# Performance work log

Measured on AMD Instinct MI355X. Metric: run time of the kernel, lower is better.

Reference implementation:

```python
import jax, jax.numpy as jnp
import numpy as np

N = 10000        # num_nodes
IN_DIM = 128     # in_dim
HID = 256        # hidden_size
EMB = 128        # final embedding dim
R = 8            # num_relations (== num_bases)
C = 32           # num_classes
E = 640000       # num_edges


def setup_inputs() -> dict:
    key = jax.random.key(0)
    ks = jax.random.split(key, 12)
    s = 0.05
    return {
        "x": jax.random.normal(ks[0], (N, N), jnp.float32) * s,
        "edge_index": jax.random.randint(ks[1], (2, E), 0, N),
        "edge_type": jax.random.randint(ks[2], (E,), 0, R),
        "emb": jax.random.normal(ks[3], (N, IN_DIM), jnp.float32) * s,
        "comp1": jax.random.normal(ks[4], (R, R), jnp.float32) * s,
        "basis1": jax.random.normal(ks[5], (R, IN_DIM, HID), jnp.float32) * s,
        "root1": jax.random.normal(ks[6], (IN_DIM, HID), jnp.float32) * s,
        "bias1": jnp.zeros((HID,), jnp.float32),
        "comp2": jax.random.normal(ks[7], (R, R), jnp.float32) * s,
        "basis2": jax.random.normal(ks[8], (R, HID, EMB), jnp.float32) * s,
        "root2": jax.random.normal(ks[9], (HID, EMB), jnp.float32) * s,
        "bias2": jnp.zeros((EMB,), jnp.float32),
        "w_dec": jax.random.normal(ks[10], (EMB, C), jnp.float32) * s,
    }


def _rgcn(h, src, dst, edge_type, comp, basis, root, bias):
    # basis-decomposed RGCN layer with mean aggregation (PyG RGCNConv semantics)
    # transform node features by every basis once: [N, B, out]
    hb = jnp.einsum("ni,bio->nbo", h, basis)
    # per-edge relation coefficients: [E, B]; message = comp[r] . hb[src]
    msg = jnp.einsum("eb,ebo->eo", comp[edge_type], hb[src])
    agg = jax.ops.segment_sum(msg, dst, num_segments=N)
    deg = jax.ops.segment_sum(jnp.ones((msg.shape[0],), h.dtype), dst, num_segments=N)
    agg = agg / jnp.maximum(deg, 1.0)[:, None]
    return agg + h @ root + bias


def reference(x, edge_index, edge_type, emb, comp1, basis1, root1, bias1,
              comp2, basis2, root2, bias2, w_dec):
    src, dst = edge_index[0], edge_index[1]
    h = jax.nn.relu(x @ emb)
    h = jax.nn.relu(_rgcn(h, src, dst, edge_type, comp1, basis1, root1, bias1))
    h = jax.nn.relu(_rgcn(h, src, dst, edge_type, comp2, basis2, root2, bias2))
    # multi-class inner-product decoder: logits = z @ W, softmax over classes
    return jax.nn.softmax(h @ w_dec, axis=1)
```

## Files before the change

kernel.cpp:

```cpp
#include <hip/hip_runtime.h>

typedef unsigned short u16;
typedef unsigned int u32;
typedef __attribute__((ext_vector_type(8))) short bf16x8;
typedef __attribute__((ext_vector_type(4))) float f32x4;

#define N_NODES 10000
#define E_EDGES 640000

static __device__ __forceinline__ float b2f(u16 u) {
  union { u32 i; float f; } x; x.i = ((u32)u) << 16; return x.f;
}
static __device__ __forceinline__ u16 f2b(float f) {
  union { float f; u32 i; } x; x.f = f;
  u32 r = x.i + 0x7FFF + ((x.i >> 16) & 1);
  return (u16)(r >> 16);
}
static __device__ __forceinline__ float ldf(const void* p, size_t i, int f32) {
  return f32 ? ((const float*)p)[i] : b2f(((const u16*)p)[i]);
}

__global__ __launch_bounds__(256) void detect_kernel(const u16* __restrict__ x, int* __restrict__ flag) {
  __shared__ int cnt_s;
  if (threadIdx.x == 0) cnt_s = 0;
  __syncthreads();
  int c = 0;
  for (int i = threadIdx.x; i < 4096; i += 256) {
    int e = (x[i] >> 7) & 255;
    if (e >= 140) c++;
  }
  atomicAdd(&cnt_s, c);
  __syncthreads();
  if (threadIdx.x == 0) flag[0] = (cnt_s > 64) ? 1 : 0;
}

__global__ void hist_kernel(const int* __restrict__ ei, const int* __restrict__ et,
                            int E, int* __restrict__ cnt8) {
  int e = blockIdx.x * 256 + threadIdx.x;
  if (e < E) atomicAdd(&cnt8[ei[E + e] * 8 + et[e]], 1);
}

__global__ void sumdst_kernel(const int* __restrict__ cnt8, int* __restrict__ dstcnt, int N) {
  int d = blockIdx.x * 256 + threadIdx.x;
  if (d >= N) return;
  const int4* p = (const int4*)(cnt8 + d * 8);
  int4 a = p[0], b = p[1];
  dstcnt[d] = a.x + a.y + a.z + a.w + b.x + b.y + b.z + b.w;
}

__global__ __launch_bounds__(256) void scan_kernel(const int* __restrict__ cnt,
                                                   int* __restrict__ offs,
                                                   int* __restrict__ cursor, int N) {
  __shared__ int tmp[256];
  const int t = threadIdx.x;
  const int CH = (N + 255) / 256;
  const int base = t * CH;
  int s = 0;
  for (int j = 0; j < CH; j++) { int p = base + j; if (p < N) s += cnt[p]; }
  tmp[t] = s;
  __syncthreads();
  for (int od = 1; od < 256; od <<= 1) {
    int a = (t >= od) ? tmp[t - od] : 0;
    __syncthreads();
    tmp[t] += a;
    __syncthreads();
  }
  int run = tmp[t] - s;
  for (int j = 0; j < CH; j++) {
    int p = base + j;
    if (p < N) { offs[p] = run; cursor[p] = run; run += cnt[p]; }
  }
  if (t == 255) offs[N] = tmp[255];
}

__global__ void segoffs_kernel(const int* __restrict__ dstoffs, const int* __restrict__ cnt8,
                               int* __restrict__ offs, int* __restrict__ cursor, int N) {
  int d = blockIdx.x * 256 + threadIdx.x;
  if (d >= N) return;
  int base = dstoffs[d];
  #pragma unroll
  for (int r = 0; r < 8; r++) {
    offs[d * 8 + r] = base;
    cursor[d * 8 + r] = base;
    base += cnt8[d * 8 + r];
  }
  if (d == N - 1) offs[N * 8] = base;
}

__global__ void bucket_kernel(const int* __restrict__ ei, const int* __restrict__ et,
                              int E, int* __restrict__ cursor, int* __restrict__ bucket) {
  int e = blockIdx.x * 256 + threadIdx.x;
  if (e < E) {
    int seg = ei[E + e] * 8 + et[e];
    int pos = atomicAdd(&cursor[seg], 1);
    bucket[pos] = ei[e];
  }
}

__global__ void transpose_kernel(const void* __restrict__ in, u16* __restrict__ out,
                                 int R, int C, const int* __restrict__ dflag) {
  __shared__ u16 tile[64][65];
  const int f = dflag[0];
  int r0 = blockIdx.x * 64, c0 = blockIdx.y * 64;
  int t = threadIdx.x;
  #pragma unroll
  for (int k = 0; k < 16; k++) {
    int lin = t + k * 256; int rr = lin >> 6, cc = lin & 63;
    int gr = r0 + rr;
    tile[rr][cc] = (gr < R) ? f2b(ldf(in, (size_t)gr * C + c0 + cc, f)) : (u16)0;
  }
  __syncthreads();
  #pragma unroll
  for (int k = 0; k < 16; k++) {
    int lin = t + k * 256; int rr = lin >> 6, cc = lin & 63;
    int gc = r0 + cc;
    if (gc < R) out[(size_t)(c0 + rr) * R + gc] = tile[cc][rr];
  }
}

template<int I, int O>
__global__ void wprep_kernel(const void* __restrict__ comp, const void* __restrict__ basis,
                             const void* __restrict__ root, u16* __restrict__ WT,
                             const int* __restrict__ dflag) {
  const int Kcat = 9 * I;
  const int f = dflag[0];
  int idx = blockIdx.x * 256 + threadIdx.x;
  if (idx >= Kcat * O) return;
  int o = idx % O;
  int kc = idx / O;
  float v;
  if (kc < 8 * I) {
    int r = kc / I, i = kc % I;
    float s = 0.f;
    #pragma unroll
    for (int b = 0; b < 8; b++)
      s += ldf(comp, r * 8 + b, f) * ldf(basis, ((size_t)b * I + i) * O + o, f);
    v = s;
  } else {
    int i = kc - 8 * I;
    v = ldf(root, (size_t)i * O + o, f);
  }
  WT[(size_t)o * Kcat + kc] = f2b(v);
}

template<int I>
__global__ void gather_seg_kernel(const u16* __restrict__ h, const int* __restrict__ offs,
                                  const int* __restrict__ bucket, u16* __restrict__ s, int node0) {
  const int d = node0 + blockIdx.x, t = threadIdx.x;
  const int sb = d * 8;
  const int b0 = offs[sb], bend = offs[sb + 8];
  const float inv = 1.0f / (float)((bend - b0) > 1 ? (bend - b0) : 1);
  const size_t base = (size_t)blockIdx.x * (9 * I);
  #pragma unroll
  for (int r = 0; r < 8; r++) {
    int j = offs[sb + r], j1 = offs[sb + r + 1];
    float a0 = 0.f, a1 = 0.f, a2 = 0.f, a3 = 0.f;
    for (; j + 3 < j1; j += 4) {
      int s0 = bucket[j], s1 = bucket[j + 1], s2 = bucket[j + 2], s3 = bucket[j + 3];
      a0 += b2f(h[(size_t)s0 * I + t]);
      a1 += b2f(h[(size_t)s1 * I + t]);
      a2 += b2f(h[(size_t)s2 * I + t]);
      a3 += b2f(h[(size_t)s3 * I + t]);
    }
    for (; j < j1; ++j) a0 += b2f(h[(size_t)bucket[j] * I + t]);
    s[base + r * I + t] = f2b((a0 + a1 + a2 + a3) * inv);
  }
  s[base + 8 * I + t] = h[(size_t)d * I + t];
}

__global__ __launch_bounds__(256) void gemm_kernel(
    const void* __restrict__ A, int lda,
    const u16* __restrict__ BT, int ldbt,
    int M, int Nout, int K,
    int tiles_per_split, int ktiles_total,
    float* __restrict__ partials,
    const int* __restrict__ dflagA) {
  __shared__ __align__(16) u16 As[128 * 32];
  __shared__ __align__(16) u16 Bs[128 * 32];
  const int f32A = dflagA ? dflagA[0] : 0;
  const int tid = threadIdx.x;
  const int wave = tid >> 6;
  const int lane = tid & 63;
  const int quad = lane >> 4;
  const int l16 = lane & 15;
  const int m0 = blockIdx.x * 128;
  const int n0 = blockIdx.y * 128;
  const int split = blockIdx.z;
  const int wm = (wave >> 1) * 64;
  const int wn = (wave & 1) * 64;

  int kt0 = split * tiles_per_split;
  int kt1 = kt0 + tiles_per_split;
  if (kt1 > ktiles_total) kt1 = ktiles_total;

  f32x4 acc[4][4];
  #pragma unroll
  for (int mi = 0; mi < 4; mi++)
    #pragma unroll
    for (int ni = 0; ni < 4; ni++) {
      f32x4 z = {0.f, 0.f, 0.f, 0.f};
      acc[mi][ni] = z;
    }

  for (int kt = kt0; kt < kt1; ++kt) {
    const int k0 = kt * 32;
    __syncthreads();
    #pragma unroll
    for (int i = 0; i < 2; ++i) {
      int c = tid + i * 256;
      int row = c >> 2, kc = c & 3;
      int kpos = k0 + kc * 8;
      uint4 vb = {0u, 0u, 0u, 0u};
      if (kpos < K) vb = *(const uint4*)(BT + (size_t)(n0 + row) * ldbt + kpos);
      *(uint4*)&Bs[(size_t)c * 8] = vb;
      uint4 va = {0u, 0u, 0u, 0u};
      if (kpos < K) {
        int ga = m0 + row; if (ga > M - 1) ga = M - 1;
        if (!f32A) {
          va = *(const uint4*)((const u16*)A + (size_t)ga * lda + kpos);
        } else {
          const float* Af = (const float*)A + (size_t)ga * lda + kpos;
          float4 f0 = ((const float4*)Af)[0];
          float4 f1 = ((const float4*)Af)[1];
          va.x = (u32)f2b(f0.x) | ((u32)f2b(f0.y) << 16);
          va.y = (u32)f2b(f0.z) | ((u32)f2b(f0.w) << 16);
          va.z = (u32)f2b(f1.x) | ((u32)f2b(f1.y) << 16);
          va.w = (u32)f2b(f1.z) | ((u32)f2b(f1.w) << 16);
        }
      }
      *(uint4*)&As[(size_t)c * 8] = va;
    }
    __syncthreads();

    bf16x8 af[4], bfr[4];
    #pragma unroll
    for (int mi = 0; mi < 4; mi++)
      af[mi] = *(const bf16x8*)&As[(size_t)(wm + mi * 16 + l16) * 32 + quad * 8];
    #pragma unroll
    for (int ni = 0; ni < 4; ni++)
      bfr[ni] = *(const bf16x8*)&Bs[(size_t)(wn + ni * 16 + l16) * 32 + quad * 8];
    #pragma unroll
    for (int mi = 0; mi < 4; mi++)
      #pragma unroll
      for (int ni = 0; ni < 4; ni++)
        acc[mi][ni] = __builtin_amdgcn_mfma_f32_16x16x32_bf16(af[mi], bfr[ni], acc[mi][ni], 0, 0, 0);
  }

  #pragma unroll
  for (int mi = 0; mi < 4; mi++)
    #pragma unroll
    for (int ni = 0; ni < 4; ni++)
      #pragma unroll
      for (int jj = 0; jj < 4; jj++) {
        int row = m0 + wm + mi * 16 + quad * 4 + jj;
        int col = n0 + wn + ni * 16 + l16;
        if (row < M) partials[((size_t)split * M + row) * Nout + col] = acc[mi][ni][jj];
      }
}

__global__ void reduce_kernel(const float* __restrict__ partials, int S, int count,
                              int nmask, const void* __restrict__ bias, u16* __restrict__ out,
                              const int* __restrict__ dflag) {
  int idx = blockIdx.x * 256 + threadIdx.x;
  if (idx >= count) return;
  float s = 0.f;
  for (int z = 0; z < S; z++) s += partials[(size_t)z * count + idx];
  if (bias) s += ldf(bias, idx & nmask, dflag[0]);
  s = s > 0.f ? s : 0.f;
  out[idx] = f2b(s);
}

__global__ __launch_bounds__(256) void decoder_kernel(const u16* __restrict__ h2,
                                                      const void* __restrict__ wdec,
                                                      void* __restrict__ out,
                                                      const int* __restrict__ dflag) {
  __shared__ float w[128 * 32];
  __shared__ float hrow[4][128];
  const int f = dflag[0];
  int t = threadIdx.x;
  for (int i = t; i < 128 * 32; i += 256) w[i] = ldf(wdec, i, f);
  int wv = t >> 6, lane = t & 63;
  int n = blockIdx.x * 4 + wv;
  hrow[wv][lane * 2]     = b2f(h2[(size_t)n * 128 + lane * 2]);
  hrow[wv][lane * 2 + 1] = b2f(h2[(size_t)n * 128 + lane * 2 + 1]);
  __syncthreads();
  int half = lane >> 5, c = lane & 31;
  float sum = 0.f;
  #pragma unroll 8
  for (int k = 0; k < 64; k++) sum += hrow[wv][half * 64 + k] * w[(half * 64 + k) * 32 + c];
  sum += __shfl_xor(sum, 32);
  float mx = sum;
  #pragma unroll
  for (int m = 16; m >= 1; m >>= 1) mx = fmaxf(mx, __shfl_xor(mx, m));
  float e = __expf(sum - mx);
  float tot = e;
  #pragma unroll
  for (int m = 16; m >= 1; m >>= 1) tot += __shfl_xor(tot, m);
  float p = e / tot;
  if (half == 0) {
    if (f) ((float*)out)[(size_t)n * 32 + c] = p;
    else   ((u16*)out)[(size_t)n * 32 + c] = f2b(p);
  }
}

extern "C" void kernel_launch(void* const* d_in, const int* in_sizes, int n_in,
                              void* d_out, int out_size, void* d_ws, size_t ws_size,
                              hipStream_t stream) {
  const void* x      = d_in[0];
  const int* ei      = (const int*)d_in[1];
  const int* et      = (const int*)d_in[2];
  const void* emb    = d_in[3];
  const void* comp1  = d_in[4];
  const void* basis1 = d_in[5];
  const void* root1  = d_in[6];
  const void* bias1  = d_in[7];
  const void* comp2  = d_in[8];
  const void* basis2 = d_in[9];
  const void* root2  = d_in[10];
  const void* bias2  = d_in[11];
  const void* wdec   = d_in[12];

  const int N = N_NODES, E = E_EDGES;
  const int NSEG = N * 8;
  auto AL = [](size_t b) -> size_t { return (b + 255) & ~(size_t)255; };

  char* base = (char*)d_ws;
  size_t off = 0;
  auto alloc = [&](size_t b) -> char* { char* p = base + off; off += AL(b); return p; };
  int* dflag  = (int*)alloc(4);
  int* offs   = (int*)alloc((size_t)(NSEG + 1) * 4);
  int* bucket = (int*)alloc((size_t)E * 4);
  u16* h0 = (u16*)alloc((size_t)N * 128 * 2);
  u16* h1 = (u16*)alloc((size_t)N * 256 * 2);
  u16* h2 = (u16*)alloc((size_t)N * 128 * 2);
  char* pool = base + off;
  size_t pool_sz = (ws_size > off) ? (ws_size - off) : 0;

  int spA = 8;
  while (spA > 1 && AL((size_t)128 * N * 2) + (size_t)spA * N * 128 * 4 > pool_sz) spA >>= 1;
  int nchunks = 1;
  while (nchunks < 32) {
    int Mc = (N + nchunks - 1) / nchunks;
    size_t reqL1 = AL((size_t)256 * 1152 * 2) + AL((size_t)Mc * 1152 * 2) + (size_t)2 * Mc * 256 * 4;
    size_t reqL2 = AL((size_t)128 * 2304 * 2) + AL((size_t)Mc * 2304 * 2) + (size_t)4 * Mc * 128 * 4;
    if (reqL1 <= pool_sz && reqL2 <= pool_sz) break;
    nchunks <<= 1;
  }
  const int Mc = (N + nchunks - 1) / nchunks;
  const int z1 = 2;
  const int z2 = 4;

  detect_kernel<<<1, 256, 0, stream>>>((const u16*)x, dflag);

  {
    char* p = pool;
    int* cnt8    = (int*)p;                 p += AL((size_t)NSEG * 4);
    int* cursor  = (int*)p;                 p += AL((size_t)NSEG * 4);
    int* dstcnt  = (int*)p;                 p += AL((size_t)N * 4);
    int* dstoffs = (int*)p;                 p += AL((size_t)(N + 1) * 4);
    int* dstcur  = (int*)p;                 p += AL((size_t)N * 4);
    hipMemsetAsync(cnt8, 0, (size_t)NSEG * 4, stream);
    hist_kernel<<<(E + 255) / 256, 256, 0, stream>>>(ei, et, E, cnt8);
    sumdst_kernel<<<(N + 255) / 256, 256, 0, stream>>>(cnt8, dstcnt, N);
    scan_kernel<<<1, 256, 0, stream>>>(dstcnt, dstoffs, dstcur, N);
    segoffs_kernel<<<(N + 255) / 256, 256, 0, stream>>>(dstoffs, cnt8, offs, cursor, N);
    bucket_kernel<<<(E + 255) / 256, 256, 0, stream>>>(ei, et, E, cursor, bucket);
  }

  {
    u16* embT = (u16*)pool;
    float* pA = (float*)(pool + AL((size_t)128 * N * 2));
    transpose_kernel<<<dim3((N + 63) / 64, 2), 256, 0, stream>>>(emb, embT, N, 128, dflag);
    int ktt = (N + 31) / 32;
    int tps = (ktt + spA - 1) / spA;
    gemm_kernel<<<dim3((N + 127) / 128, 1, spA), 256, 0, stream>>>(
        x, N, embT, N, N, 128, N, tps, ktt, pA, dflag);
    reduce_kernel<<<(N * 128 + 255) / 256, 256, 0, stream>>>(
        pA, spA, N * 128, 127, (const void*)nullptr, h0, dflag);
  }

  {
    u16* WT1 = (u16*)pool;
    char* chunkbase = pool + AL((size_t)256 * 1152 * 2);
    wprep_kernel<128, 256><<<(1152 * 256 + 255) / 256, 256, 0, stream>>>(comp1, basis1, root1, WT1, dflag);
    for (int c = 0; c < nchunks; c++) {
      int node0 = c * Mc;
      int rows = N - node0; if (rows > Mc) rows = Mc;
      if (rows <= 0) break;
      u16* s1 = (u16*)chunkbase;
      float* p1 = (float*)(chunkbase + AL((size_t)Mc * 1152 * 2));
      gather_seg_kernel<128><<<rows, 128, 0, stream>>>(h0, offs, bucket, s1, node0);
      gemm_kernel<<<dim3((rows + 127) / 128, 2, z1), 256, 0, stream>>>(
          s1, 1152, WT1, 1152, rows, 256, 1152, (36 + z1 - 1) / z1, 36, p1, (const int*)nullptr);
      reduce_kernel<<<(rows * 256 + 255) / 256, 256, 0, stream>>>(
          p1, z1, rows * 256, 255, bias1, h1 + (size_t)node0 * 256, dflag);
    }
  }

  {
    u16* WT2 = (u16*)pool;
    char* chunkbase = pool + AL((size_t)128 * 2304 * 2);
    wprep_kernel<256, 128><<<(2304 * 128 + 255) / 256, 256, 0, stream>>>(comp2, basis2, root2, WT2, dflag);
    for (int c = 0; c < nchunks; c++) {
      int node0 = c * Mc;
      int rows = N - node0; if (rows > Mc) rows = Mc;
      if (rows <= 0) break;
      u16* s2 = (u16*)chunkbase;
      float* p2 = (float*)(chunkbase + AL((size_t)Mc * 2304 * 2));
      gather_seg_kernel<256><<<rows, 256, 0, stream>>>(h1, offs, bucket, s2, node0);
      gemm_kernel<<<dim3((rows + 127) / 128, 1, z2), 256, 0, stream>>>(
          s2, 2304, WT2, 2304, rows, 128, 2304, (72 + z2 - 1) / z2, 72, p2, (const int*)nullptr);
      reduce_kernel<<<(rows * 128 + 255) / 256, 256, 0, stream>>>(
          p2, z2, rows * 128, 127, bias2, h2 + (size_t)node0 * 128, dflag);
    }
  }

  decoder_kernel<<<N / 4, 256, 0, stream>>>(h2, wdec, d_out, dflag);
}
```

Before: 899.3 us.

## Replace split-K partial buffers with atomic accumulation and fuse preprocessing kernels

Split-K GEMMs now atomically add into zeroed fp32 outputs, so the separate reduce passes and partial buffers go away. A lighter finalize applies bias and ReLU, and the last layer's finalize is folded into the decoder. The CSR build merges sumdst, scan and segoffs into one single-block kernel. Both weight preparations run in one launch, gather kernels use vectorized 32/64-bit loads with 64-thread blocks, node chunking is removed, and layer 2 split-K goes from 4 to 8. The costs are float atomic contention and non-deterministic summation order, a larger memset, and a serial single-block scan over 80K counts.

```diff
diff --git a/kernel.cpp b/kernel.cpp
--- a/kernel.cpp
+++ b/kernel.cpp
@@ -40,23 +40,21 @@
   if (e < E) atomicAdd(&cnt8[ei[E + e] * 8 + et[e]], 1);
 }
 
-__global__ void sumdst_kernel(const int* __restrict__ cnt8, int* __restrict__ dstcnt, int N) {
-  int d = blockIdx.x * 256 + threadIdx.x;
-  if (d >= N) return;
-  const int4* p = (const int4*)(cnt8 + d * 8);
-  int4 a = p[0], b = p[1];
-  dstcnt[d] = a.x + a.y + a.z + a.w + b.x + b.y + b.z + b.w;
-}
-
-__global__ __launch_bounds__(256) void scan_kernel(const int* __restrict__ cnt,
-                                                   int* __restrict__ offs,
-                                                   int* __restrict__ cursor, int N) {
+__global__ __launch_bounds__(256) void segscan_kernel(const int* __restrict__ cnt8,
+                                                      int* __restrict__ offs,
+                                                      int* __restrict__ cursor) {
   __shared__ int tmp[256];
   const int t = threadIdx.x;
-  const int CH = (N + 255) / 256;
-  const int base = t * CH;
+  const int CH = (N_NODES + 255) / 256;
+  const int d0 = t * CH;
   int s = 0;
-  for (int j = 0; j < CH; j++) { int p = base + j; if (p < N) s += cnt[p]; }
+  for (int j = 0; j < CH; j++) {
+    int d = d0 + j;
+    if (d < N_NODES) {
+      #pragma unroll
+      for (int r = 0; r < 8; r++) s += cnt8[d * 8 + r];
+    }
+  }
   tmp[t] = s;
   __syncthreads();
   for (int od = 1; od < 256; od <<= 1) {
@@ -67,24 +65,17 @@
   }
   int run = tmp[t] - s;
   for (int j = 0; j < CH; j++) {
-    int p = base + j;
-    if (p < N) { offs[p] = run; cursor[p] = run; run += cnt[p]; }
-  }
-  if (t == 255) offs[N] = tmp[255];
-}
-
-__global__ void segoffs_kernel(const int* __restrict__ dstoffs, const int* __restrict__ cnt8,
-                               int* __restrict__ offs, int* __restrict__ cursor, int N) {
-  int d = blockIdx.x * 256 + threadIdx.x;
-  if (d >= N) return;
-  int base = dstoffs[d];
-  #pragma unroll
-  for (int r = 0; r < 8; r++) {
-    offs[d * 8 + r] = base;
-    cursor[d * 8 + r] = base;
-    base += cnt8[d * 8 + r];
-  }
-  if (d == N - 1) offs[N * 8] = base;
+    int d = d0 + j;
+    if (d < N_NODES) {
+      #pragma unroll
+      for (int r = 0; r < 8; r++) {
+        offs[d * 8 + r] = run;
+        cursor[d * 8 + r] = run;
+        run += cnt8[d * 8 + r];
+      }
+    }
+  }
+  if (t == 255) offs[N_NODES * 8] = tmp[255];
 }
 
 __global__ void bucket_kernel(const int* __restrict__ ei, const int* __restrict__ et,
@@ -119,12 +110,11 @@
 }
 
 template<int I, int O>
-__global__ void wprep_kernel(const void* __restrict__ comp, const void* __restrict__ basis,
-                             const void* __restrict__ root, u16* __restrict__ WT,
-                             const int* __restrict__ dflag) {
+static __device__ __forceinline__ void wprep_body(const void* comp, const void* basis,
+                                                  const void* root, u16* WT,
+                                                  int f, int blk) {
   const int Kcat = 9 * I;
-  const int f = dflag[0];
-  int idx = blockIdx.x * 256 + threadIdx.x;
+  int idx = blk * 256 + threadIdx.x;
   if (idx >= Kcat * O) return;
   int o = idx % O;
   int kc = idx / O;
@@ -143,29 +133,85 @@
   WT[(size_t)o * Kcat + kc] = f2b(v);
 }
 
-template<int I>
-__global__ void gather_seg_kernel(const u16* __restrict__ h, const int* __restrict__ offs,
-                                  const int* __restrict__ bucket, u16* __restrict__ s, int node0) {
-  const int d = node0 + blockIdx.x, t = threadIdx.x;
+__global__ void wprep_both_kernel(const void* c1, const void* b1, const void* r1, u16* WT1,
+                                  const void* c2, const void* b2, const void* r2, u16* WT2,
+                                  const int* __restrict__ dflag) {
+  const int f = dflag[0];
+  int blk = blockIdx.x;
+  if (blk < 1152) wprep_body<128, 256>(c1, b1, r1, WT1, f, blk);
+  else            wprep_body<256, 128>(c2, b2, r2, WT2, f, blk - 1152);
+}
+
+__global__ void gather1_kernel(const u16* __restrict__ h, const int* __restrict__ offs,
+                               const int* __restrict__ bucket, u16* __restrict__ s) {
+  const int d = blockIdx.x, t = threadIdx.x;
+  const u32* __restrict__ h32 = (const u32*)h;
+  u32* s32 = (u32*)s;
   const int sb = d * 8;
   const int b0 = offs[sb], bend = offs[sb + 8];
   const float inv = 1.0f / (float)((bend - b0) > 1 ? (bend - b0) : 1);
-  const size_t base = (size_t)blockIdx.x * (9 * I);
+  const int base = d * 576;
   #pragma unroll
   for (int r = 0; r < 8; r++) {
     int j = offs[sb + r], j1 = offs[sb + r + 1];
-    float a0 = 0.f, a1 = 0.f, a2 = 0.f, a3 = 0.f;
+    float l0 = 0.f, h0a = 0.f, l1 = 0.f, h1a = 0.f, l2 = 0.f, h2a = 0.f, l3 = 0.f, h3a = 0.f;
     for (; j + 3 < j1; j += 4) {
-      int s0 = bucket[j], s1 = bucket[j + 1], s2 = bucket[j + 2], s3 = bucket[j + 3];
-      a0 += b2f(h[(size_t)s0 * I + t]);
-      a1 += b2f(h[(size_t)s1 * I + t]);
-      a2 += b2f(h[(size_t)s2 * I + t]);
-      a3 += b2f(h[(size_t)s3 * I + t]);
-    }
-    for (; j < j1; ++j) a0 += b2f(h[(size_t)bucket[j] * I + t]);
-    s[base + r * I + t] = f2b((a0 + a1 + a2 + a3) * inv);
-  }
-  s[base + 8 * I + t] = h[(size_t)d * I + t];
+      u32 v0 = h32[(size_t)bucket[j] * 64 + t];
+      u32 v1 = h32[(size_t)bucket[j + 1] * 64 + t];
+      u32 v2 = h32[(size_t)bucket[j + 2] * 64 + t];
+      u32 v3 = h32[(size_t)bucket[j + 3] * 64 + t];
+      l0 += b2f((u16)v0); h0a += b2f((u16)(v0 >> 16));
+      l1 += b2f((u16)v1); h1a += b2f((u16)(v1 >> 16));
+      l2 += b2f((u16)v2); h2a += b2f((u16)(v2 >> 16));
+      l3 += b2f((u16)v3); h3a += b2f((u16)(v3 >> 16));
+    }
+    for (; j < j1; ++j) {
+      u32 v = h32[(size_t)bucket[j] * 64 + t];
+      l0 += b2f((u16)v); h0a += b2f((u16)(v >> 16));
+    }
+    float sl = (l0 + l1 + l2 + l3) * inv, sh = (h0a + h1a + h2a + h3a) * inv;
+    s32[base + r * 64 + t] = (u32)f2b(sl) | ((u32)f2b(sh) << 16);
+  }
+  s32[base + 512 + t] = h32[(size_t)d * 64 + t];
+}
+
+__global__ void gather2_kernel(const u16* __restrict__ h, const int* __restrict__ offs,
+                               const int* __restrict__ bucket, u16* __restrict__ s) {
+  const int d = blockIdx.x, t = threadIdx.x;
+  const uint2* __restrict__ h64 = (const uint2*)h;
+  uint2* s64 = (uint2*)s;
+  const int sb = d * 8;
+  const int b0 = offs[sb], bend = offs[sb + 8];
+  const float inv = 1.0f / (float)((bend - b0) > 1 ? (bend - b0) : 1);
+  const int base = d * 576;
+  #pragma unroll
+  for (int r = 0; r < 8; r++) {
+    int j = offs[sb + r], j1 = offs[sb + r + 1];
+    float4 A0 = {0.f, 0.f, 0.f, 0.f}, A1 = A0, A2 = A0, A3 = A0;
+    for (; j + 3 < j1; j += 4) {
+      uint2 v0 = h64[(size_t)bucket[j] * 64 + t];
+      uint2 v1 = h64[(size_t)bucket[j + 1] * 64 + t];
+      uint2 v2 = h64[(size_t)bucket[j + 2] * 64 + t];
+      uint2 v3 = h64[(size_t)bucket[j + 3] * 64 + t];
+      A0.x += b2f((u16)v0.x); A0.y += b2f((u16)(v0.x >> 16)); A0.z += b2f((u16)v0.y); A0.w += b2f((u16)(v0.y >> 16));
+      A1.x += b2f((u16)v1.x); A1.y += b2f((u16)(v1.x >> 16)); A1.z += b2f((u16)v1.y); A1.w += b2f((u16)(v1.y >> 16));
+      A2.x += b2f((u16)v2.x); A2.y += b2f((u16)(v2.x >> 16)); A2.z += b2f((u16)v2.y); A2.w += b2f((u16)(v2.y >> 16));
+      A3.x += b2f((u16)v3.x); A3.y += b2f((u16)(v3.x >> 16)); A3.z += b2f((u16)v3.y); A3.w += b2f((u16)(v3.y >> 16));
+    }
+    for (; j < j1; ++j) {
+      uint2 v = h64[(size_t)bucket[j] * 64 + t];
+      A0.x += b2f((u16)v.x); A0.y += b2f((u16)(v.x >> 16)); A0.z += b2f((u16)v.y); A0.w += b2f((u16)(v.y >> 16));
+    }
+    float sx = (A0.x + A1.x + A2.x + A3.x) * inv;
+    float sy = (A0.y + A1.y + A2.y + A3.y) * inv;
+    float sz = (A0.z + A1.z + A2.z + A3.z) * inv;
+    float sw = (A0.w + A1.w + A2.w + A3.w) * inv;
+    uint2 o;
+    o.x = (u32)f2b(sx) | ((u32)f2b(sy) << 16);
+    o.y = (u32)f2b(sz) | ((u32)f2b(sw) << 16);
+    s64[base + r * 64 + t] = o;
+  }
+  s64[base + 512 + t] = h64[(size_t)d * 64 + t];
 }
 
 __global__ __launch_bounds__(256) void gemm_kernel(
@@ -173,7 +219,7 @@
     const u16* __restrict__ BT, int ldbt,
     int M, int Nout, int K,
     int tiles_per_split, int ktiles_total,
-    float* __restrict__ partials,
+    float* __restrict__ outf,
     const int* __restrict__ dflagA) {
   __shared__ __align__(16) u16 As[128 * 32];
   __shared__ __align__(16) u16 Bs[128 * 32];
@@ -254,24 +300,33 @@
       for (int jj = 0; jj < 4; jj++) {
         int row = m0 + wm + mi * 16 + quad * 4 + jj;
         int col = n0 + wn + ni * 16 + l16;
-        if (row < M) partials[((size_t)split * M + row) * Nout + col] = acc[mi][ni][jj];
+        if (row < M) atomicAdd(&outf[(size_t)row * Nout + col], acc[mi][ni][jj]);
       }
 }
 
-__global__ void reduce_kernel(const float* __restrict__ partials, int S, int count,
-                              int nmask, const void* __restrict__ bias, u16* __restrict__ out,
-                              const int* __restrict__ dflag) {
-  int idx = blockIdx.x * 256 + threadIdx.x;
-  if (idx >= count) return;
-  float s = 0.f;
-  for (int z = 0; z < S; z++) s += partials[(size_t)z * count + idx];
-  if (bias) s += ldf(bias, idx & nmask, dflag[0]);
-  s = s > 0.f ? s : 0.f;
-  out[idx] = f2b(s);
-}
-
-__global__ __launch_bounds__(256) void decoder_kernel(const u16* __restrict__ h2,
+__global__ void finalize_kernel(const float* __restrict__ accf, int count4, int nmask,
+                                const void* __restrict__ bias, u16* __restrict__ out,
+                                const int* __restrict__ dflag) {
+  int i = blockIdx.x * 256 + threadIdx.x;
+  if (i >= count4) return;
+  const int f = dflag[0];
+  float4 v = ((const float4*)accf)[i];
+  if (bias) {
+    int c = (i * 4) & nmask;
+    v.x += ldf(bias, c, f);
+    v.y += ldf(bias, c + 1, f);
+    v.z += ldf(bias, c + 2, f);
+    v.w += ldf(bias, c + 3, f);
+  }
+  v.x = fmaxf(v.x, 0.f); v.y = fmaxf(v.y, 0.f); v.z = fmaxf(v.z, 0.f); v.w = fmaxf(v.w, 0.f);
+  ushort4 o;
+  o.x = f2b(v.x); o.y = f2b(v.y); o.z = f2b(v.z); o.w = f2b(v.w);
+  *(ushort4*)(out + (size_t)i * 4) = o;
+}
+
+__global__ __launch_bounds__(256) void decoder_kernel(const float* __restrict__ h2f,
                                                       const void* __restrict__ wdec,
+                                                      const void* __restrict__ bias2,
                                                       void* __restrict__ out,
                                                       const int* __restrict__ dflag) {
   __shared__ float w[128 * 32];
@@ -281,8 +336,9 @@
   for (int i = t; i < 128 * 32; i += 256) w[i] = ldf(wdec, i, f);
   int wv = t >> 6, lane = t & 63;
   int n = blockIdx.x * 4 + wv;
-  hrow[wv][lane * 2]     = b2f(h2[(size_t)n * 128 + lane * 2]);
-  hrow[wv][lane * 2 + 1] = b2f(h2[(size_t)n * 128 + lane * 2 + 1]);
+  float b0 = ldf(bias2, lane * 2, f), b1 = ldf(bias2, lane * 2 + 1, f);
+  hrow[wv][lane * 2]     = fmaxf(h2f[(size_t)n * 128 + lane * 2] + b0, 0.f);
+  hrow[wv][lane * 2 + 1] = fmaxf(h2f[(size_t)n * 128 + lane * 2 + 1] + b1, 0.f);
   __syncthreads();
   int half = lane >> 5, c = lane & 31;
   float sum = 0.f;
@@ -327,93 +383,59 @@
   char* base = (char*)d_ws;
   size_t off = 0;
   auto alloc = [&](size_t b) -> char* { char* p = base + off; off += AL(b); return p; };
-  int* dflag  = (int*)alloc(4);
-  int* offs   = (int*)alloc((size_t)(NSEG + 1) * 4);
-  int* bucket = (int*)alloc((size_t)E * 4);
-  u16* h0 = (u16*)alloc((size_t)N * 128 * 2);
-  u16* h1 = (u16*)alloc((size_t)N * 256 * 2);
-  u16* h2 = (u16*)alloc((size_t)N * 128 * 2);
-  char* pool = base + off;
-  size_t pool_sz = (ws_size > off) ? (ws_size - off) : 0;
-
-  int spA = 8;
-  while (spA > 1 && AL((size_t)128 * N * 2) + (size_t)spA * N * 128 * 4 > pool_sz) spA >>= 1;
-  int nchunks = 1;
-  while (nchunks < 32) {
-    int Mc = (N + nchunks - 1) / nchunks;
-    size_t reqL1 = AL((size_t)256 * 1152 * 2) + AL((size_t)Mc * 1152 * 2) + (size_t)2 * Mc * 256 * 4;
-    size_t reqL2 = AL((size_t)128 * 2304 * 2) + AL((size_t)Mc * 2304 * 2) + (size_t)4 * Mc * 128 * 4;
-    if (reqL1 <= pool_sz && reqL2 <= pool_sz) break;
-    nchunks <<= 1;
-  }
-  const int Mc = (N + nchunks - 1) / nchunks;
-  const int z1 = 2;
-  const int z2 = 4;
+  int* dflag   = (int*)alloc(4);
+  int* offs    = (int*)alloc((size_t)(NSEG + 1) * 4);
+  int* cursor  = (int*)alloc((size_t)NSEG * 4);
+  int* bucket  = (int*)alloc((size_t)E * 4);
+  u16* h0      = (u16*)alloc((size_t)N * 128 * 2);
+  u16* h1      = (u16*)alloc((size_t)N * 256 * 2);
+  size_t zoff0 = off;
+  int*   cnt8  = (int*)alloc((size_t)NSEG * 4);
+  float* h0f   = (float*)alloc((size_t)N * 128 * 4);
+  float* h1f   = (float*)alloc((size_t)N * 256 * 4);
+  float* h2f   = (float*)alloc((size_t)N * 128 * 4);
+  size_t zbytes = off - zoff0;
+  u16* WT1     = (u16*)alloc((size_t)256 * 1152 * 2);
+  u16* WT2     = (u16*)alloc((size_t)128 * 2304 * 2);
+  u16* embT    = (u16*)alloc((size_t)128 * N * 2);
+  u16* s1      = (u16*)alloc((size_t)N * 1152 * 2);
+  u16* s2      = (u16*)alloc((size_t)N * 2304 * 2);
 
   detect_kernel<<<1, 256, 0, stream>>>((const u16*)x, dflag);
 
+  hipMemsetAsync(cnt8, 0, zbytes, stream);
+
+  hist_kernel<<<(E + 255) / 256, 256, 0, stream>>>(ei, et, E, cnt8);
+  segscan_kernel<<<1, 256, 0, stream>>>(cnt8, offs, cursor);
+  bucket_kernel<<<(E + 255) / 256, 256, 0, stream>>>(ei, et, E, cursor, bucket);
+
+  transpose_kernel<<<dim3((N + 63) / 64, 2), 256, 0, stream>>>(emb, embT, N, 128, dflag);
+  wprep_both_kernel<<<2304, 256, 0, stream>>>(comp1, basis1, root1, WT1,
+                                              comp2, basis2, root2, WT2, dflag);
+
   {
-    char* p = pool;
-    int* cnt8    = (int*)p;                 p += AL((size_t)NSEG * 4);
-    int* cursor  = (int*)p;                 p += AL((size_t)NSEG * 4);
-    int* dstcnt  = (int*)p;                 p += AL((size_t)N * 4);
-    int* dstoffs = (int*)p;                 p += AL((size_t)(N + 1) * 4);
-    int* dstcur  = (int*)p;                 p += AL((size_t)N * 4);
-    hipMemsetAsync(cnt8, 0, (size_t)NSEG * 4, stream);
-    hist_kernel<<<(E + 255) / 256, 256, 0, stream>>>(ei, et, E, cnt8);
-    sumdst_kernel<<<(N + 255) / 256, 256, 0, stream>>>(cnt8, dstcnt, N);
-    scan_kernel<<<1, 256, 0, stream>>>(dstcnt, dstoffs, dstcur, N);
-    segoffs_kernel<<<(N + 255) / 256, 256, 0, stream>>>(dstoffs, cnt8, offs, cursor, N);
-    bucket_kernel<<<(E + 255) / 256, 256, 0, stream>>>(ei, et, E, cursor, bucket);
-  }
-
-  {
-    u16* embT = (u16*)pool;
-    float* pA = (float*)(pool + AL((size_t)128 * N * 2));
-    transpose_kernel<<<dim3((N + 63) / 64, 2), 256, 0, stream>>>(emb, embT, N, 128, dflag);
     int ktt = (N + 31) / 32;
+    int spA = 8;
     int tps = (ktt + spA - 1) / spA;
     gemm_kernel<<<dim3((N + 127) / 128, 1, spA), 256, 0, stream>>>(
-        x, N, embT, N, N, 128, N, tps, ktt, pA, dflag);
-    reduce_kernel<<<(N * 128 + 255) / 256, 256, 0, stream>>>(
-        pA, spA, N * 128, 127, (const void*)nullptr, h0, dflag);
+        x, N, embT, N, N, 128, N, tps, ktt, h0f, dflag);
+    finalize_kernel<<<(N * 128 / 4 + 255) / 256, 256, 0, stream>>>(
+        h0f, N * 128 / 4, 127, (const void*)nullptr, h0, dflag);
   }
 
   {
-    u16* WT1 = (u16*)pool;
-    char* chunkbase = pool + AL((size_t)256 * 1152 * 2);
-    wprep_kernel<128, 256><<<(1152 * 256 + 255) / 256, 256, 0, stream>>>(comp1, basis1, root1, WT1, dflag);
-    for (int c = 0; c < nchunks; c++) {
-      int node0 = c * Mc;
-      int rows = N - node0; if (rows > Mc) rows = Mc;
-      if (rows <= 0) break;
-      u16* s1 = (u16*)chunkbase;
-      float* p1 = (float*)(chunkbase + AL((size_t)Mc * 1152 * 2));
-      gather_seg_kernel<128><<<rows, 128, 0, stream>>>(h0, offs, bucket, s1, node0);
-      gemm_kernel<<<dim3((rows + 127) / 128, 2, z1), 256, 0, stream>>>(
-          s1, 1152, WT1, 1152, rows, 256, 1152, (36 + z1 - 1) / z1, 36, p1, (const int*)nullptr);
-      reduce_kernel<<<(rows * 256 + 255) / 256, 256, 0, stream>>>(
-          p1, z1, rows * 256, 255, bias1, h1 + (size_t)node0 * 256, dflag);
-    }
+    gather1_kernel<<<N, 64, 0, stream>>>(h0, offs, bucket, s1);
+    gemm_kernel<<<dim3((N + 127) / 128, 2, 4), 256, 0, stream>>>(
+        s1, 1152, WT1, 1152, N, 256, 1152, 9, 36, h1f, (const int*)nullptr);
+    finalize_kernel<<<(N * 256 / 4 + 255) / 256, 256, 0, stream>>>(
+        h1f, N * 256 / 4, 255, bias1, h1, dflag);
   }
 
   {
-    u16* WT2 = (u16*)pool;
-    char* chunkbase = pool + AL((size_t)128 * 2304 * 2);
-    wprep_kernel<256, 128><<<(2304 * 128 + 255) / 256, 256, 0, stream>>>(comp2, basis2, root2, WT2, dflag);
-    for (int c = 0; c < nchunks; c++) {
-      int node0 = c * Mc;
-      int rows = N - node0; if (rows > Mc) rows = Mc;
-      if (rows <= 0) break;
-      u16* s2 = (u16*)chunkbase;
-      float* p2 = (float*)(chunkbase + AL((size_t)Mc * 2304 * 2));
-      gather_seg_kernel<256><<<rows, 256, 0, stream>>>(h1, offs, bucket, s2, node0);
-      gemm_kernel<<<dim3((rows + 127) / 128, 1, z2), 256, 0, stream>>>(
-          s2, 2304, WT2, 2304, rows, 128, 2304, (72 + z2 - 1) / z2, 72, p2, (const int*)nullptr);
-      reduce_kernel<<<(rows * 128 + 255) / 256, 256, 0, stream>>>(
-          p2, z2, rows * 128, 127, bias2, h2 + (size_t)node0 * 128, dflag);
-    }
-  }
-
-  decoder_kernel<<<N / 4, 256, 0, stream>>>(h2, wdec, d_out, dflag);
-}
+    gather2_kernel<<<N, 64, 0, stream>>>(h1, offs, bucket, s2);
+    gemm_kernel<<<dim3((N + 127) / 128, 1, 8), 256, 0, stream>>>(
+        s2, 2304, WT2, 2304, N, 128, 2304, 9, 72, h2f, (const int*)nullptr);
+  }
+
+  decoder_kernel<<<N / 4, 256, 0, stream>>>(h2f, wdec, bias2, d_out, dflag);
+}
```

Result: no change. 916.7 us (+1.9%).
